# Performance work log

Measured on AMD Instinct MI355X. Metric: run time of the kernel, lower is better.

## Reference

```python
import jax, jax.numpy as jnp
import numpy as np

B, H, S, DH = 1, 16, 4096, 128
D_MODEL = H * DH  # 2048


def setup_inputs() -> dict:
    key = jax.random.key(0)
    kq, kk, kv = jax.random.split(key, 3)
    q = jax.random.normal(kq, (B, H, S, DH), dtype=jnp.float32)
    k = jax.random.normal(kk, (B, H, S, DH), dtype=jnp.float32)
    v = jax.random.normal(kv, (B, H, S, DH), dtype=jnp.float32)
    # causal mask: 1 where attending is allowed, 0 elsewhere (masked_fill on ==0)
    attn_mask = jnp.tril(jnp.ones((S, S), dtype=jnp.int32))[None, None, :, :]
    return {"q": q, "k": k, "v": v, "seq_length": S, "attn_mask": attn_mask}


def reference(q, k, v, seq_length, attn_mask):
    # q,k,v: [1, H, S, DH]; attn_mask: [1, 1, S, S] (0 = masked)
    scale = 1.0 / jnp.sqrt(jnp.asarray(q.shape[-1], dtype=q.dtype))
    att = jnp.einsum("bhqd,bhkd->bhqk", q, k) * scale  # [1,H,S,S]
    mask = attn_mask[:, :, :seq_length, :seq_length]
    att = jnp.where(mask == 0, jnp.asarray(-jnp.inf, dtype=att.dtype), att)
    att = jax.nn.softmax(att, axis=-1)
    y = jnp.einsum("bhqk,bhkd->bhqd", att, v)  # [1,H,S,DH]
    # transpose(1,2) -> [1,S,H,DH] -> view(S, d_model)
    y = jnp.transpose(y, (0, 2, 1, 3)).reshape(seq_length, H * DH)
    return y
```

## Files before the change

kernel.cpp:

```cpp
#include <hip/hip_runtime.h>

#define HH 16
#define SS 4096
#define DHD 128
#define BR 64
#define BC 64
#define LDQ 144
#define LDV 68
#define LDPT 72
#define LDOS 136
#define DM  (HH * DHD)

typedef __bf16 bf16x8_t __attribute__((ext_vector_type(8)));
typedef __bf16 bf16x4_t __attribute__((ext_vector_type(4)));
typedef float  f32x4_t  __attribute__((ext_vector_type(4)));

#define BAR() asm volatile("s_waitcnt lgkmcnt(0)\n\ts_barrier" ::: "memory")

__device__ __forceinline__ f32x4_t vmax4(f32x4_t a, f32x4_t b) {
    f32x4_t r;
    r[0] = fmaxf(a[0], b[0]); r[1] = fmaxf(a[1], b[1]);
    r[2] = fmaxf(a[2], b[2]); r[3] = fmaxf(a[3], b[3]);
    return r;
}

__global__ __launch_bounds__(256, 3)
void fa_fwd(const float* __restrict__ q, const float* __restrict__ k,
            const float* __restrict__ v, float* __restrict__ out)
{
    const int L = blockIdx.x;
    const int h = L & 15;
    const int qt = 63 - (L >> 4);

    const int tid  = threadIdx.x;
    const int wave = tid >> 6;
    const int lane = tid & 63;
    const int l16  = lane & 15;
    const int quad = lane >> 4;
    const int rK   = tid >> 5;
    const int c4   = tid & 31;
    const int dbase = (wave & 1) * 64;
    const int rbase = (wave >> 1) * 32;

    __shared__ __align__(16) char smem[45056];
    unsigned short* k_s  = (unsigned short*)smem;
    unsigned short* vt_s = (unsigned short*)(smem + 18432);
    unsigned short* pT_s = (unsigned short*)(smem + 35840);
    float* os = (float*)smem;

    const size_t hoff = (size_t)h * SS * DHD;
    const float* qh = q + hoff;
    const float* kh = k + hoff;
    const float* vh = v + hoff;

    float4 kreg[8];
    float  vreg[8][4];
    auto issue = [&](int j) {
        const float* kb = kh + (size_t)j * BC * DHD;
        #pragma unroll
        for (int i = 0; i < 8; ++i)
            kreg[i] = ((const float4*)(kb + (size_t)(rK + i * 8) * DHD))[c4];
        const float* vb = vh + (size_t)j * BC * DHD + dbase + lane;
        #pragma unroll
        for (int p = 0; p < 8; ++p) {
            const float* vp = vb + (size_t)(rbase + p * 4) * DHD;
            vreg[p][0] = vp[0];
            vreg[p][1] = vp[DHD];
            vreg[p][2] = vp[2 * DHD];
            vreg[p][3] = vp[3 * DHD];
        }
    };

    const float scale = 0.088388347648318447f * 1.4426950408889634f;
    issue(0);

    #pragma unroll
    for (int i = 0; i < 8; ++i) {
        int idx = tid + i * 256;
        int r   = idx >> 5;
        int cc  = idx & 31;
        float4 val = ((const float4*)(qh + (size_t)(qt * BR + r) * DHD))[cc];
        bf16x4_t bb;
        bb[0] = (__bf16)(val.x * scale); bb[1] = (__bf16)(val.y * scale);
        bb[2] = (__bf16)(val.z * scale); bb[3] = (__bf16)(val.w * scale);
        *(bf16x4_t*)&k_s[r * LDQ + cc * 4] = bb;
    }
    __syncthreads();

    bf16x8_t qf[4];
    #pragma unroll
    for (int kc = 0; kc < 4; ++kc)
        qf[kc] = *(const bf16x8_t*)
            &k_s[(wave * 16 + l16) * LDQ + kc * 32 + quad * 8];

    f32x4_t oacc[8];
    #pragma unroll
    for (int mt = 0; mt < 8; ++mt) oacc[mt] = (f32x4_t)(0.0f);
    float mi = -INFINITY, li = 0.0f;

    const int q_local = wave * 16 + l16;

    for (int j = 0; j <= qt; ++j) {
        BAR();
        #pragma unroll
        for (int i = 0; i < 8; ++i) {
            bf16x4_t bb;
            bb[0] = (__bf16)kreg[i].x; bb[1] = (__bf16)kreg[i].y;
            bb[2] = (__bf16)kreg[i].z; bb[3] = (__bf16)kreg[i].w;
            *(bf16x4_t*)&k_s[(rK + i * 8) * LDQ + c4 * 4] = bb;
        }
        #pragma unroll
        for (int p = 0; p < 8; ++p) {
            bf16x4_t bb;
            bb[0] = (__bf16)vreg[p][0]; bb[1] = (__bf16)vreg[p][1];
            bb[2] = (__bf16)vreg[p][2]; bb[3] = (__bf16)vreg[p][3];
            *(bf16x4_t*)&vt_s[(dbase + lane) * LDV + rbase + p * 4] = bb;
        }
        if (j < qt) issue(j + 1);
        BAR();

        f32x4_t sa[4];
        #pragma unroll
        for (int mt = 0; mt < 4; ++mt) sa[mt] = (f32x4_t)(0.0f);
        #pragma unroll
        for (int kc = 0; kc < 4; ++kc)
            #pragma unroll
            for (int mt = 0; mt < 4; ++mt) {
                bf16x8_t kf = *(const bf16x8_t*)
                    &k_s[(mt * 16 + l16) * LDQ + kc * 32 + quad * 8];
                sa[mt] = __builtin_amdgcn_mfma_f32_16x16x32_bf16(kf, qf[kc], sa[mt], 0, 0, 0);
            }

        if (j == qt) {
            #pragma unroll
            for (int mt = 0; mt < 4; ++mt)
                #pragma unroll
                for (int r = 0; r < 4; ++r)
                    if (mt * 16 + quad * 4 + r > q_local) sa[mt][r] = -INFINITY;
        }

        f32x4_t mv = vmax4(vmax4(sa[0], sa[1]), vmax4(sa[2], sa[3]));
        float mx = fmaxf(fmaxf(mv[0], mv[1]), fmaxf(mv[2], mv[3]));
        mx = fmaxf(mx, __shfl_xor(mx, 16));
        mx = fmaxf(mx, __shfl_xor(mx, 32));
        const bool skip = __all((int)(mx <= mi + 8.0f)) != 0;
        const float mnew = skip ? mi : fmaxf(mi, mx);
        bf16x4_t pkv[4];
        #pragma unroll
        for (int mt = 0; mt < 4; ++mt) {
            #pragma unroll
            for (int r = 0; r < 4; ++r)
                sa[mt][r] = __builtin_amdgcn_exp2f(sa[mt][r] - mnew);
            pkv[mt][0] = (__bf16)sa[mt][0]; pkv[mt][1] = (__bf16)sa[mt][1];
            pkv[mt][2] = (__bf16)sa[mt][2]; pkv[mt][3] = (__bf16)sa[mt][3];
        }
        f32x4_t sv = sa[0] + sa[1] + sa[2] + sa[3];
        float rs = (sv[0] + sv[1]) + (sv[2] + sv[3]);
        rs += __shfl_xor(rs, 16);
        rs += __shfl_xor(rs, 32);
        if (skip) {
            li += rs;
        } else {
            float a = __builtin_amdgcn_exp2f(mi - mnew);
            mi = mnew;
            li = li * a + rs;
            #pragma unroll
            for (int mt = 0; mt < 8; ++mt) {
                oacc[mt][0] *= a; oacc[mt][1] *= a;
                oacc[mt][2] *= a; oacc[mt][3] *= a;
            }
        }

        #pragma unroll
        for (int mt = 0; mt < 4; ++mt)
            *(bf16x4_t*)&pT_s[(wave * 16 + l16) * LDPT + mt * 16 + quad * 4] = pkv[mt];

        #pragma unroll
        for (int kc = 0; kc < 2; ++kc) {
            bf16x8_t pb = *(const bf16x8_t*)
                &pT_s[(wave * 16 + l16) * LDPT + kc * 32 + quad * 8];
            #pragma unroll
            for (int mt = 0; mt < 8; ++mt) {
                bf16x4_t vlo = *(const bf16x4_t*)
                    &vt_s[(mt * 16 + l16) * LDV + kc * 32 + quad * 8];
                bf16x4_t vhi = *(const bf16x4_t*)
                    &vt_s[(mt * 16 + l16) * LDV + kc * 32 + quad * 8 + 4];
                bf16x8_t vf = __builtin_shufflevector(vlo, vhi, 0,1,2,3,4,5,6,7);
                oacc[mt] = __builtin_amdgcn_mfma_f32_16x16x32_bf16(vf, pb, oacc[mt], 0, 0, 0);
            }
        }
    }

    __syncthreads();
    float inv = 1.0f / li;
    #pragma unroll
    for (int mt = 0; mt < 8; ++mt)
        #pragma unroll
        for (int r = 0; r < 4; ++r)
            os[(wave * 16 + l16) * LDOS + mt * 16 + quad * 4 + r] = oacc[mt][r] * inv;
    __syncthreads();
    #pragma unroll
    for (int p = 0; p < 8; ++p) {
        int row = p * 8 + rK;
        float4 f4 = *(const float4*)&os[row * LDOS + c4 * 4];
        *(float4*)&out[(size_t)(qt * BR + row) * DM + h * DHD + c4 * 4] = f4;
    }
}

extern "C" void kernel_launch(void* const* d_in, const int* in_sizes, int n_in,
                              void* d_out, int out_size, void* d_ws, size_t ws_size,
                              hipStream_t stream) {
    const float* q = (const float*)d_in[0];
    const float* k = (const float*)d_in[1];
    const float* v = (const float*)d_in[2];
    float* out = (float*)d_out;
    fa_fwd<<<dim3((SS / BR) * HH), dim3(256), 0, stream>>>(q, k, v, out);
}
```

Before: 321.0 us.

## Pair complementary causal query tiles per block and double-buffer K/V in LDS

Each block now processes two query tiles, g and 63-g, so every block does the same amount of causal work. The grid is halved to 512 blocks. K/V tiles are double-buffered in LDS: the next tile is committed while the current one is consumed, leaving one barrier per iteration, and the prefetch runs across the boundary between the two tiles. MFMA sections are wrapped in s_setprio. The cost is more LDS (about 80 KB), which lowers the occupancy bound to 2 blocks per CU, and each block now runs twice as long.

```diff
diff --git a/kernel.cpp b/kernel.cpp
--- a/kernel.cpp
+++ b/kernel.cpp
@@ -24,13 +24,14 @@
     return r;
 }
 
-__global__ __launch_bounds__(256, 3)
+__global__ __launch_bounds__(256, 2)
 void fa_fwd(const float* __restrict__ q, const float* __restrict__ k,
             const float* __restrict__ v, float* __restrict__ out)
 {
     const int L = blockIdx.x;
     const int h = L & 15;
-    const int qt = 63 - (L >> 4);
+    const int g = L >> 4;
+    const int qts[2] = { g, 63 - g };
 
     const int tid  = threadIdx.x;
     const int wave = tid >> 6;
@@ -42,10 +43,8 @@
     const int dbase = (wave & 1) * 64;
     const int rbase = (wave >> 1) * 32;
 
-    __shared__ __align__(16) char smem[45056];
-    unsigned short* k_s  = (unsigned short*)smem;
-    unsigned short* vt_s = (unsigned short*)(smem + 18432);
-    unsigned short* pT_s = (unsigned short*)(smem + 35840);
+    __shared__ __align__(16) char smem[80896];
+    unsigned short* pT_s = (unsigned short*)(smem + 71680);
     float* os = (float*)smem;
 
     const size_t hoff = (size_t)h * SS * DHD;
@@ -70,140 +69,166 @@
             vreg[p][3] = vp[3 * DHD];
         }
     };
-
-    const float scale = 0.088388347648318447f * 1.4426950408889634f;
-    issue(0);
-
-    #pragma unroll
-    for (int i = 0; i < 8; ++i) {
-        int idx = tid + i * 256;
-        int r   = idx >> 5;
-        int cc  = idx & 31;
-        float4 val = ((const float4*)(qh + (size_t)(qt * BR + r) * DHD))[cc];
-        bf16x4_t bb;
-        bb[0] = (__bf16)(val.x * scale); bb[1] = (__bf16)(val.y * scale);
-        bb[2] = (__bf16)(val.z * scale); bb[3] = (__bf16)(val.w * scale);
-        *(bf16x4_t*)&k_s[r * LDQ + cc * 4] = bb;
-    }
-    __syncthreads();
-
-    bf16x8_t qf[4];
-    #pragma unroll
-    for (int kc = 0; kc < 4; ++kc)
-        qf[kc] = *(const bf16x8_t*)
-            &k_s[(wave * 16 + l16) * LDQ + kc * 32 + quad * 8];
-
-    f32x4_t oacc[8];
-    #pragma unroll
-    for (int mt = 0; mt < 8; ++mt) oacc[mt] = (f32x4_t)(0.0f);
-    float mi = -INFINITY, li = 0.0f;
-
-    const int q_local = wave * 16 + l16;
-
-    for (int j = 0; j <= qt; ++j) {
-        BAR();
+    auto commit = [&](int b) {
+        unsigned short* ks = (unsigned short*)(smem + b * 18432);
+        unsigned short* vs = (unsigned short*)(smem + 36864 + b * 17408);
         #pragma unroll
         for (int i = 0; i < 8; ++i) {
             bf16x4_t bb;
             bb[0] = (__bf16)kreg[i].x; bb[1] = (__bf16)kreg[i].y;
             bb[2] = (__bf16)kreg[i].z; bb[3] = (__bf16)kreg[i].w;
-            *(bf16x4_t*)&k_s[(rK + i * 8) * LDQ + c4 * 4] = bb;
+            *(bf16x4_t*)&ks[(rK + i * 8) * LDQ + c4 * 4] = bb;
         }
         #pragma unroll
         for (int p = 0; p < 8; ++p) {
             bf16x4_t bb;
             bb[0] = (__bf16)vreg[p][0]; bb[1] = (__bf16)vreg[p][1];
             bb[2] = (__bf16)vreg[p][2]; bb[3] = (__bf16)vreg[p][3];
-            *(bf16x4_t*)&vt_s[(dbase + lane) * LDV + rbase + p * 4] = bb;
-        }
-        if (j < qt) issue(j + 1);
+            *(bf16x4_t*)&vs[(dbase + lane) * LDV + rbase + p * 4] = bb;
+        }
+    };
+
+    const float scale = 0.088388347648318447f * 1.4426950408889634f;
+    issue(0);
+
+    for (int t = 0; t < 2; ++t) {
+        const int qt = qts[t];
+        __syncthreads();
+        unsigned short* q_s = (unsigned short*)(smem + 18432);
+        #pragma unroll
+        for (int i = 0; i < 8; ++i) {
+            int idx = tid + i * 256;
+            int r   = idx >> 5;
+            int cc  = idx & 31;
+            float4 val = ((const float4*)(qh + (size_t)(qt * BR + r) * DHD))[cc];
+            bf16x4_t bb;
+            bb[0] = (__bf16)(val.x * scale); bb[1] = (__bf16)(val.y * scale);
+            bb[2] = (__bf16)(val.z * scale); bb[3] = (__bf16)(val.w * scale);
+            *(bf16x4_t*)&q_s[r * LDQ + cc * 4] = bb;
+        }
+        __syncthreads();
+
+        bf16x8_t qf[4];
+        #pragma unroll
+        for (int kc = 0; kc < 4; ++kc)
+            qf[kc] = *(const bf16x8_t*)
+                &q_s[(wave * 16 + l16) * LDQ + kc * 32 + quad * 8];
+
+        f32x4_t oacc[8];
+        #pragma unroll
+        for (int mt = 0; mt < 8; ++mt) oacc[mt] = (f32x4_t)(0.0f);
+        float mi = -INFINITY, li = 0.0f;
+
+        const int q_local = wave * 16 + l16;
+
+        commit(0);
+        if (qt >= 1)     issue(1);
+        else if (t == 0) issue(0);
         BAR();
 
-        f32x4_t sa[4];
-        #pragma unroll
-        for (int mt = 0; mt < 4; ++mt) sa[mt] = (f32x4_t)(0.0f);
-        #pragma unroll
-        for (int kc = 0; kc < 4; ++kc)
+        for (int j = 0; j <= qt; ++j) {
+            const int br = j & 1;
+            unsigned short* ks = (unsigned short*)(smem + br * 18432);
+            unsigned short* vs = (unsigned short*)(smem + 36864 + br * 17408);
+
+            f32x4_t sa[4];
+            #pragma unroll
+            for (int mt = 0; mt < 4; ++mt) sa[mt] = (f32x4_t)(0.0f);
+            __builtin_amdgcn_s_setprio(1);
+            #pragma unroll
+            for (int kc = 0; kc < 4; ++kc)
+                #pragma unroll
+                for (int mt = 0; mt < 4; ++mt) {
+                    bf16x8_t kf = *(const bf16x8_t*)
+                        &ks[(mt * 16 + l16) * LDQ + kc * 32 + quad * 8];
+                    sa[mt] = __builtin_amdgcn_mfma_f32_16x16x32_bf16(kf, qf[kc], sa[mt], 0, 0, 0);
+                }
+            __builtin_amdgcn_s_setprio(0);
+
+            if (j < qt) {
+                commit(br ^ 1);
+                if (j + 2 <= qt) issue(j + 2);
+                else if (t == 0) issue(0);
+            }
+
+            if (j == qt) {
+                #pragma unroll
+                for (int mt = 0; mt < 4; ++mt)
+                    #pragma unroll
+                    for (int r = 0; r < 4; ++r)
+                        if (mt * 16 + quad * 4 + r > q_local) sa[mt][r] = -INFINITY;
+            }
+
+            f32x4_t mv = vmax4(vmax4(sa[0], sa[1]), vmax4(sa[2], sa[3]));
+            float mx = fmaxf(fmaxf(mv[0], mv[1]), fmaxf(mv[2], mv[3]));
+            mx = fmaxf(mx, __shfl_xor(mx, 16));
+            mx = fmaxf(mx, __shfl_xor(mx, 32));
+            const bool skip = __all((int)(mx <= mi + 8.0f)) != 0;
+            const float mnew = skip ? mi : fmaxf(mi, mx);
+            bf16x4_t pkv[4];
             #pragma unroll
             for (int mt = 0; mt < 4; ++mt) {
-                bf16x8_t kf = *(const bf16x8_t*)
-                    &k_s[(mt * 16 + l16) * LDQ + kc * 32 + quad * 8];
-                sa[mt] = __builtin_amdgcn_mfma_f32_16x16x32_bf16(kf, qf[kc], sa[mt], 0, 0, 0);
-            }
-
-        if (j == qt) {
+                #pragma unroll
+                for (int r = 0; r < 4; ++r)
+                    sa[mt][r] = __builtin_amdgcn_exp2f(sa[mt][r] - mnew);
+                pkv[mt][0] = (__bf16)sa[mt][0]; pkv[mt][1] = (__bf16)sa[mt][1];
+                pkv[mt][2] = (__bf16)sa[mt][2]; pkv[mt][3] = (__bf16)sa[mt][3];
+            }
+            f32x4_t sv = sa[0] + sa[1] + sa[2] + sa[3];
+            float rs = (sv[0] + sv[1]) + (sv[2] + sv[3]);
+            rs += __shfl_xor(rs, 16);
+            rs += __shfl_xor(rs, 32);
+            if (skip) {
+                li += rs;
+            } else {
+                float a = __builtin_amdgcn_exp2f(mi - mnew);
+                mi = mnew;
+                li = li * a + rs;
+                #pragma unroll
+                for (int mt = 0; mt < 8; ++mt) {
+                    oacc[mt][0] *= a; oacc[mt][1] *= a;
+                    oacc[mt][2] *= a; oacc[mt][3] *= a;
+                }
+            }
+
             #pragma unroll
             for (int mt = 0; mt < 4; ++mt)
-                #pragma unroll
-                for (int r = 0; r < 4; ++r)
-                    if (mt * 16 + quad * 4 + r > q_local) sa[mt][r] = -INFINITY;
-        }
-
-        f32x4_t mv = vmax4(vmax4(sa[0], sa[1]), vmax4(sa[2], sa[3]));
-        float mx = fmaxf(fmaxf(mv[0], mv[1]), fmaxf(mv[2], mv[3]));
-        mx = fmaxf(mx, __shfl_xor(mx, 16));
-        mx = fmaxf(mx, __shfl_xor(mx, 32));
-        const bool skip = __all((int)(mx <= mi + 8.0f)) != 0;
-        const float mnew = skip ? mi : fmaxf(mi, mx);
-        bf16x4_t pkv[4];
-        #pragma unroll
-        for (int mt = 0; mt < 4; ++mt) {
+                *(bf16x4_t*)&pT_s[(wave * 16 + l16) * LDPT + mt * 16 + quad * 4] = pkv[mt];
+
+            __builtin_amdgcn_s_setprio(1);
+            #pragma unroll
+            for (int kc = 0; kc < 2; ++kc) {
+                bf16x8_t pb = *(const bf16x8_t*)
+                    &pT_s[(wave * 16 + l16) * LDPT + kc * 32 + quad * 8];
+                #pragma unroll
+                for (int mt = 0; mt < 8; ++mt) {
+                    bf16x4_t vlo = *(const bf16x4_t*)
+                        &vs[(mt * 16 + l16) * LDV + kc * 32 + quad * 8];
+                    bf16x4_t vhi = *(const bf16x4_t*)
+                        &vs[(mt * 16 + l16) * LDV + kc * 32 + quad * 8 + 4];
+                    bf16x8_t vf = __builtin_shufflevector(vlo, vhi, 0,1,2,3,4,5,6,7);
+                    oacc[mt] = __builtin_amdgcn_mfma_f32_16x16x32_bf16(vf, pb, oacc[mt], 0, 0, 0);
+                }
+            }
+            __builtin_amdgcn_s_setprio(0);
+
+            BAR();
+        }
+
+        __syncthreads();
+        float inv = 1.0f / li;
+        #pragma unroll
+        for (int mt = 0; mt < 8; ++mt)
             #pragma unroll
             for (int r = 0; r < 4; ++r)
-                sa[mt][r] = __builtin_amdgcn_exp2f(sa[mt][r] - mnew);
-            pkv[mt][0] = (__bf16)sa[mt][0]; pkv[mt][1] = (__bf16)sa[mt][1];
-            pkv[mt][2] = (__bf16)sa[mt][2]; pkv[mt][3] = (__bf16)sa[mt][3];
-        }
-        f32x4_t sv = sa[0] + sa[1] + sa[2] + sa[3];
-        float rs = (sv[0] + sv[1]) + (sv[2] + sv[3]);
-        rs += __shfl_xor(rs, 16);
-        rs += __shfl_xor(rs, 32);
-        if (skip) {
-            li += rs;
-        } else {
-            float a = __builtin_amdgcn_exp2f(mi - mnew);
-            mi = mnew;
-            li = li * a + rs;
-            #pragma unroll
-            for (int mt = 0; mt < 8; ++mt) {
-                oacc[mt][0] *= a; oacc[mt][1] *= a;
-                oacc[mt][2] *= a; oacc[mt][3] *= a;
-            }
-        }
-
-        #pragma unroll
-        for (int mt = 0; mt < 4; ++mt)
-            *(bf16x4_t*)&pT_s[(wave * 16 + l16) * LDPT + mt * 16 + quad * 4] = pkv[mt];
-
-        #pragma unroll
-        for (int kc = 0; kc < 2; ++kc) {
-            bf16x8_t pb = *(const bf16x8_t*)
-                &pT_s[(wave * 16 + l16) * LDPT + kc * 32 + quad * 8];
-            #pragma unroll
-            for (int mt = 0; mt < 8; ++mt) {
-                bf16x4_t vlo = *(const bf16x4_t*)
-                    &vt_s[(mt * 16 + l16) * LDV + kc * 32 + quad * 8];
-                bf16x4_t vhi = *(const bf16x4_t*)
-                    &vt_s[(mt * 16 + l16) * LDV + kc * 32 + quad * 8 + 4];
-                bf16x8_t vf = __builtin_shufflevector(vlo, vhi, 0,1,2,3,4,5,6,7);
-                oacc[mt] = __builtin_amdgcn_mfma_f32_16x16x32_bf16(vf, pb, oacc[mt], 0, 0, 0);
-            }
-        }
-    }
-
-    __syncthreads();
-    float inv = 1.0f / li;
-    #pragma unroll
-    for (int mt = 0; mt < 8; ++mt)
-        #pragma unroll
-        for (int r = 0; r < 4; ++r)
-            os[(wave * 16 + l16) * LDOS + mt * 16 + quad * 4 + r] = oacc[mt][r] * inv;
-    __syncthreads();
-    #pragma unroll
-    for (int p = 0; p < 8; ++p) {
-        int row = p * 8 + rK;
-        float4 f4 = *(const float4*)&os[row * LDOS + c4 * 4];
-        *(float4*)&out[(size_t)(qt * BR + row) * DM + h * DHD + c4 * 4] = f4;
+                os[(wave * 16 + l16) * LDOS + mt * 16 + quad * 4 + r] = oacc[mt][r] * inv;
+        __syncthreads();
+        #pragma unroll
+        for (int p = 0; p < 8; ++p) {
+            int row = p * 8 + rK;
+            float4 f4 = *(const float4*)&os[row * LDOS + c4 * 4];
+            *(float4*)&out[(size_t)(qt * BR + row) * DM + h * DHD + c4 * 4] = f4;
+        }
     }
 }
 
@@ -214,5 +239,5 @@
     const float* k = (const float*)d_in[1];
     const float* v = (const float*)d_in[2];
     float* out = (float*)d_out;
-    fa_fwd<<<dim3((SS / BR) * HH), dim3(256), 0, stream>>>(q, k, v, out);
+    fa_fwd<<<dim3((SS / BR / 2) * HH), dim3(256), 0, stream>>>(q, k, v, out);
 }
```

Result: slower. 350.1 us (+9.1%).

## Double query tile to 128 rows with 512-thread blocks sharing K/V tiles

Applied to the files above, without the earlier changes.

Each block now handles 128 query rows with eight waves, so every K/V tile loaded and converted to bf16 in shared memory serves twice as many queries. This cuts global K/V traffic and conversion work per query. Q moves to its own shared-memory stride, causal masking now covers the last two KV tiles, and the output is written back in two halves through shared memory. The block ordering is changed to pair heavy and light causal tiles, and s_setprio is raised around the MFMA sections. In exchange there are fewer blocks, more shared memory per block and lower occupancy, and the larger causal diagonal does more masked work.

```diff
diff --git a/kernel.cpp b/kernel.cpp
--- a/kernel.cpp
+++ b/kernel.cpp
@@ -3,9 +3,10 @@
 #define HH 16
 #define SS 4096
 #define DHD 128
-#define BR 64
+#define BR 128
 #define BC 64
 #define LDQ 144
+#define LDQS 136
 #define LDV 68
 #define LDPT 72
 #define LDOS 136
@@ -24,13 +25,15 @@
     return r;
 }
 
-__global__ __launch_bounds__(256, 3)
+__global__ __launch_bounds__(512, 2)
 void fa_fwd(const float* __restrict__ q, const float* __restrict__ k,
             const float* __restrict__ v, float* __restrict__ out)
 {
-    const int L = blockIdx.x;
-    const int h = L & 15;
-    const int qt = 63 - (L >> 4);
+    const int L  = blockIdx.x;
+    const int h  = L & 15;
+    const int i5 = L >> 4;
+    const int qt = (i5 < 16) ? (31 - i5) : (i5 - 16);
+    const int jmax = 2 * qt + 1;
 
     const int tid  = threadIdx.x;
     const int wave = tid >> 6;
@@ -40,12 +43,13 @@
     const int rK   = tid >> 5;
     const int c4   = tid & 31;
     const int dbase = (wave & 1) * 64;
-    const int rbase = (wave >> 1) * 32;
-
-    __shared__ __align__(16) char smem[45056];
+    const int rbase = (wave >> 1) * 16;
+
+    __shared__ __align__(16) char smem[54272];
     unsigned short* k_s  = (unsigned short*)smem;
     unsigned short* vt_s = (unsigned short*)(smem + 18432);
     unsigned short* pT_s = (unsigned short*)(smem + 35840);
+    unsigned short* q_s  = (unsigned short*)smem;
     float* os = (float*)smem;
 
     const size_t hoff = (size_t)h * SS * DHD;
@@ -53,16 +57,16 @@
     const float* kh = k + hoff;
     const float* vh = v + hoff;
 
-    float4 kreg[8];
-    float  vreg[8][4];
+    float4 kreg[4];
+    float  vreg[4][4];
     auto issue = [&](int j) {
         const float* kb = kh + (size_t)j * BC * DHD;
         #pragma unroll
-        for (int i = 0; i < 8; ++i)
-            kreg[i] = ((const float4*)(kb + (size_t)(rK + i * 8) * DHD))[c4];
+        for (int i = 0; i < 4; ++i)
+            kreg[i] = ((const float4*)(kb + (size_t)(rK + i * 16) * DHD))[c4];
         const float* vb = vh + (size_t)j * BC * DHD + dbase + lane;
         #pragma unroll
-        for (int p = 0; p < 8; ++p) {
+        for (int p = 0; p < 4; ++p) {
             const float* vp = vb + (size_t)(rbase + p * 4) * DHD;
             vreg[p][0] = vp[0];
             vreg[p][1] = vp[DHD];
@@ -70,58 +74,60 @@
             vreg[p][3] = vp[3 * DHD];
         }
     };
+    auto commit = [&]() {
+        #pragma unroll
+        for (int i = 0; i < 4; ++i) {
+            bf16x4_t bb;
+            bb[0] = (__bf16)kreg[i].x; bb[1] = (__bf16)kreg[i].y;
+            bb[2] = (__bf16)kreg[i].z; bb[3] = (__bf16)kreg[i].w;
+            *(bf16x4_t*)&k_s[(rK + i * 16) * LDQ + c4 * 4] = bb;
+        }
+        #pragma unroll
+        for (int p = 0; p < 4; ++p) {
+            bf16x4_t bb;
+            bb[0] = (__bf16)vreg[p][0]; bb[1] = (__bf16)vreg[p][1];
+            bb[2] = (__bf16)vreg[p][2]; bb[3] = (__bf16)vreg[p][3];
+            *(bf16x4_t*)&vt_s[(dbase + lane) * LDV + rbase + p * 4] = bb;
+        }
+    };
 
     const float scale = 0.088388347648318447f * 1.4426950408889634f;
     issue(0);
 
     #pragma unroll
     for (int i = 0; i < 8; ++i) {
-        int idx = tid + i * 256;
+        int idx = tid + i * 512;
         int r   = idx >> 5;
         int cc  = idx & 31;
         float4 val = ((const float4*)(qh + (size_t)(qt * BR + r) * DHD))[cc];
         bf16x4_t bb;
         bb[0] = (__bf16)(val.x * scale); bb[1] = (__bf16)(val.y * scale);
         bb[2] = (__bf16)(val.z * scale); bb[3] = (__bf16)(val.w * scale);
-        *(bf16x4_t*)&k_s[r * LDQ + cc * 4] = bb;
+        *(bf16x4_t*)&q_s[r * LDQS + cc * 4] = bb;
     }
     __syncthreads();
 
+    const int q_local = wave * 16 + l16;
     bf16x8_t qf[4];
     #pragma unroll
     for (int kc = 0; kc < 4; ++kc)
-        qf[kc] = *(const bf16x8_t*)
-            &k_s[(wave * 16 + l16) * LDQ + kc * 32 + quad * 8];
+        qf[kc] = *(const bf16x8_t*)&q_s[q_local * LDQS + kc * 32 + quad * 8];
 
     f32x4_t oacc[8];
     #pragma unroll
     for (int mt = 0; mt < 8; ++mt) oacc[mt] = (f32x4_t)(0.0f);
     float mi = -INFINITY, li = 0.0f;
 
-    const int q_local = wave * 16 + l16;
-
-    for (int j = 0; j <= qt; ++j) {
+    for (int j = 0; j <= jmax; ++j) {
         BAR();
-        #pragma unroll
-        for (int i = 0; i < 8; ++i) {
-            bf16x4_t bb;
-            bb[0] = (__bf16)kreg[i].x; bb[1] = (__bf16)kreg[i].y;
-            bb[2] = (__bf16)kreg[i].z; bb[3] = (__bf16)kreg[i].w;
-            *(bf16x4_t*)&k_s[(rK + i * 8) * LDQ + c4 * 4] = bb;
-        }
-        #pragma unroll
-        for (int p = 0; p < 8; ++p) {
-            bf16x4_t bb;
-            bb[0] = (__bf16)vreg[p][0]; bb[1] = (__bf16)vreg[p][1];
-            bb[2] = (__bf16)vreg[p][2]; bb[3] = (__bf16)vreg[p][3];
-            *(bf16x4_t*)&vt_s[(dbase + lane) * LDV + rbase + p * 4] = bb;
-        }
-        if (j < qt) issue(j + 1);
+        commit();
+        if (j < jmax) issue(j + 1);
         BAR();
 
         f32x4_t sa[4];
         #pragma unroll
         for (int mt = 0; mt < 4; ++mt) sa[mt] = (f32x4_t)(0.0f);
+        __builtin_amdgcn_s_setprio(1);
         #pragma unroll
         for (int kc = 0; kc < 4; ++kc)
             #pragma unroll
@@ -130,13 +136,15 @@
                     &k_s[(mt * 16 + l16) * LDQ + kc * 32 + quad * 8];
                 sa[mt] = __builtin_amdgcn_mfma_f32_16x16x32_bf16(kf, qf[kc], sa[mt], 0, 0, 0);
             }
-
-        if (j == qt) {
+        __builtin_amdgcn_s_setprio(0);
+
+        if (j >= 2 * qt) {
+            const int off = (j - 2 * qt) * 64;
             #pragma unroll
             for (int mt = 0; mt < 4; ++mt)
                 #pragma unroll
                 for (int r = 0; r < 4; ++r)
-                    if (mt * 16 + quad * 4 + r > q_local) sa[mt][r] = -INFINITY;
+                    if (off + mt * 16 + quad * 4 + r > q_local) sa[mt][r] = -INFINITY;
         }
 
         f32x4_t mv = vmax4(vmax4(sa[0], sa[1]), vmax4(sa[2], sa[3]));
@@ -173,12 +181,13 @@
 
         #pragma unroll
         for (int mt = 0; mt < 4; ++mt)
-            *(bf16x4_t*)&pT_s[(wave * 16 + l16) * LDPT + mt * 16 + quad * 4] = pkv[mt];
-
+            *(bf16x4_t*)&pT_s[q_local * LDPT + mt * 16 + quad * 4] = pkv[mt];
+
+        __builtin_amdgcn_s_setprio(1);
         #pragma unroll
         for (int kc = 0; kc < 2; ++kc) {
             bf16x8_t pb = *(const bf16x8_t*)
-                &pT_s[(wave * 16 + l16) * LDPT + kc * 32 + quad * 8];
+                &pT_s[q_local * LDPT + kc * 32 + quad * 8];
             #pragma unroll
             for (int mt = 0; mt < 8; ++mt) {
                 bf16x4_t vlo = *(const bf16x4_t*)
@@ -189,21 +198,29 @@
                 oacc[mt] = __builtin_amdgcn_mfma_f32_16x16x32_bf16(vf, pb, oacc[mt], 0, 0, 0);
             }
         }
+        __builtin_amdgcn_s_setprio(0);
     }
 
     __syncthreads();
-    float inv = 1.0f / li;
-    #pragma unroll
-    for (int mt = 0; mt < 8; ++mt)
-        #pragma unroll
-        for (int r = 0; r < 4; ++r)
-            os[(wave * 16 + l16) * LDOS + mt * 16 + quad * 4 + r] = oacc[mt][r] * inv;
-    __syncthreads();
-    #pragma unroll
-    for (int p = 0; p < 8; ++p) {
-        int row = p * 8 + rK;
-        float4 f4 = *(const float4*)&os[row * LDOS + c4 * 4];
-        *(float4*)&out[(size_t)(qt * BR + row) * DM + h * DHD + c4 * 4] = f4;
+    const float inv = 1.0f / li;
+    #pragma unroll
+    for (int half = 0; half < 2; ++half) {
+        if ((wave >> 2) == half) {
+            const int orow = (wave & 3) * 16 + l16;
+            #pragma unroll
+            for (int mt = 0; mt < 8; ++mt)
+                #pragma unroll
+                for (int r = 0; r < 4; ++r)
+                    os[orow * LDOS + mt * 16 + quad * 4 + r] = oacc[mt][r] * inv;
+        }
+        __syncthreads();
+        #pragma unroll
+        for (int p = 0; p < 4; ++p) {
+            int row = p * 16 + rK;
+            float4 f4 = *(const float4*)&os[row * LDOS + c4 * 4];
+            *(float4*)&out[(size_t)(qt * BR + half * 64 + row) * DM + h * DHD + c4 * 4] = f4;
+        }
+        __syncthreads();
     }
 }
 
@@ -214,5 +231,5 @@
     const float* k = (const float*)d_in[1];
     const float* v = (const float*)d_in[2];
     float* out = (float*)d_out;
-    fa_fwd<<<dim3((SS / BR) * HH), dim3(256), 0, stream>>>(q, k, v, out);
+    fa_fwd<<<dim3((SS / BR) * HH), dim3(512), 0, stream>>>(q, k, v, out);
 }
```

Result: slower. 331.3 us (+3.2%).
